# Optimization experiments

Hardware: AMD Instinct MI355X
Metric: run time of the kernel (lower is better)

## Reference

```python
import jax, jax.numpy as jnp
import numpy as np

B, T, D = 64, 512, 1024
H0, H1 = 1024, 1024

def setup_inputs() -> dict:
    key = jax.random.key(0)
    k1, k2, k3 = jax.random.split(key, 3)
    # scale weights ~ 1/sqrt(fan_in) so tanh doesn't saturate
    s0 = 1.0 / np.sqrt(H0 + D)
    s1 = 1.0 / np.sqrt(H1 + H0)
    return {
        "x": jax.random.normal(k1, (B, T, D), dtype=jnp.float32),
        "W0": jax.random.normal(k2, (H0 + D, H0), dtype=jnp.float32) * s0,
        "b0": jnp.zeros((H0,), dtype=jnp.float32),
        "W1": jax.random.normal(k3, (H1 + H0, H1), dtype=jnp.float32) * s1,
        "b1": jnp.zeros((H1,), dtype=jnp.float32),
    }

def reference(x, W0, b0, W1, b1):
    batch = x.shape[0]
    h0_init = jnp.zeros((batch, W0.shape[1]), dtype=x.dtype)
    h1_init = jnp.zeros((batch, W1.shape[1]), dtype=x.dtype)

    def step(carry, xt):
        h0, h1 = carry
        # layer 0: concat(prev hidden, input) -> dense -> tanh
        h0 = jnp.tanh(jnp.concatenate([h0, xt], axis=-1) @ W0 + b0)
        # layer 1 consumes layer 0 output
        h1 = jnp.tanh(jnp.concatenate([h1, h0], axis=-1) @ W1 + b1)
        return (h0, h1), h1

    xs = jnp.swapaxes(x, 0, 1)  # [T, B, D] time-major for scan
    (h0_f, h1_f), ys = jax.lax.scan(step, (h0_init, h1_init), xs)
    outputs = jnp.swapaxes(ys, 0, 1)  # [B, T, H1]
    final_state = jnp.concatenate([h0_f, h1_f], axis=-1)  # [B, H0+H1]
    return outputs, final_state
```

## Files before the change

### kernel.cpp

```cpp
#include <hip/hip_runtime.h>
#include <cmath>


typedef unsigned short u16;
typedef unsigned int   u32;
typedef unsigned long long u64;
typedef __bf16 bf16x8 __attribute__((ext_vector_type(8)));
typedef u16    u16x8  __attribute__((ext_vector_type(8)));
typedef u16    u16x4  __attribute__((ext_vector_type(4)));
typedef float  f32x4  __attribute__((ext_vector_type(4)));

constexpr int BB = 64;
constexpr int TT = 512;
constexpr size_t SLOT   = (size_t)64 * 1024;
constexpr size_t SLAB_B = SLOT * 2;

constexpr size_t OFF_W0T = 262144;
constexpr size_t OFF_W1T = OFF_W0T + (size_t)1024 * 2048 * 2;
constexpr size_t OFF_R   = OFF_W1T + (size_t)1024 * 2048 * 2;

constexpr int LDS_REQ = 159744;

__device__ inline u16 f2bf(float f) { return __builtin_bit_cast(u16, (__bf16)f); }
__device__ inline float bf2f(u16 v) { return (float)__builtin_bit_cast(__bf16, v); }
__device__ inline float fast_tanh(float x) {
  x = fminf(15.f, fmaxf(-15.f, x));
  float e = __expf(2.f * x);
  return (e - 1.f) * __builtin_amdgcn_rcpf(e + 1.f);
}

__global__ void zero_flags(unsigned* f) {
  int i = blockIdx.x * 256 + threadIdx.x;
  if (i < 3 * 512 * 32) f[i] = 0;
}

__global__ void transpose_w(const float* __restrict__ W0,
                            const float* __restrict__ W1,
                            u16* __restrict__ wt_base) {
  __shared__ float tile[64][65];
  int bi  = blockIdx.x;
  int mat = bi >> 9;
  int t   = bi & 511;
  int tk = t & 31, tn = t >> 5;
  const float* W = mat ? W1 : W0;
  u16* Wt = wt_base + (size_t)mat * 1024 * 2048;
  int K0 = tk * 64, N0 = tn * 64;
  int tid = threadIdx.x;
  {
    int c4 = (tid & 15) * 4;
    int r  = tid >> 4;
    for (int i = 0; i < 4; ++i) {
      int kl = r + i * 16;
      float4 v = *(const float4*)(W + (size_t)(K0 + kl) * 1024 + N0 + c4);
      tile[kl][c4 + 0] = v.x; tile[kl][c4 + 1] = v.y;
      tile[kl][c4 + 2] = v.z; tile[kl][c4 + 3] = v.w;
    }
  }
  __syncthreads();
  {
    int nl = tid >> 3;
    int kc = (tid & 7) * 8;
    for (int pass = 0; pass < 2; ++pass) {
      int n = nl + pass * 32;
      u16x8 o;
      #pragma unroll
      for (int z = 0; z < 8; ++z) o[z] = f2bf(tile[kc + z][n]);
      *(u16x8*)(Wt + (size_t)(N0 + n) * 2048 + K0 + kc) = o;
    }
  }
}

__global__ void xconv(const float* __restrict__ x, u16* __restrict__ xb) {
  int bi = blockIdx.x;
  int b = bi >> 9, t = bi & 511;
  const float* src = x + ((size_t)b * TT + t) * 1024;
  u16* dst = xb + ((size_t)t * BB + b) * 1024;
  int i = threadIdx.x * 4;
  float4 v = *(const float4*)(src + i);
  u16x4 o; o[0] = f2bf(v.x); o[1] = f2bf(v.y); o[2] = f2bf(v.z); o[3] = f2bf(v.w);
  *(u16x4*)(dst + i) = o;
}

__device__ inline void poll1(unsigned* p) {
  while (__hip_atomic_load(p, __ATOMIC_RELAXED, __HIP_MEMORY_SCOPE_SYSTEM) == 0u)
    __builtin_amdgcn_s_sleep(1);
}

template<bool COHA>
__device__ inline void mm8(const u16* Abase, const u16* bp, size_t aoff,
                           int gbase, int n15, f32x4& acc0, f32x4& acc1) {
  const u16* ap = Abase + aoff;
  #pragma unroll
  for (int ks = 0; ks < 8; ++ks) {
    bf16x8 a;
    if constexpr (COHA) {
      u64 lo = __hip_atomic_load((u64*)(ap + ks * 32),     __ATOMIC_RELAXED, __HIP_MEMORY_SCOPE_SYSTEM);
      u64 hi = __hip_atomic_load((u64*)(ap + ks * 32 + 4), __ATOMIC_RELAXED, __HIP_MEMORY_SCOPE_SYSTEM);
      union { u64 q2[2]; bf16x8 v; } un; un.q2[0] = lo; un.q2[1] = hi;
      a = un.v;
    } else {
      a = __builtin_bit_cast(bf16x8, *(const u16x8*)(ap + ks * 32));
    }
    int g = (gbase + 4 * ks) ^ n15;
    bf16x8 b0 = __builtin_bit_cast(bf16x8, *(const u16x8*)(bp + g * 8));
    bf16x8 b1 = __builtin_bit_cast(bf16x8, *(const u16x8*)(bp + 16 * 1024 + g * 8));
    acc0 = __builtin_amdgcn_mfma_f32_16x16x32_bf16(a, b0, acc0, 0, 0, 0);
    acc1 = __builtin_amdgcn_mfma_f32_16x16x32_bf16(a, b1, acc1, 0, 0, 0);
  }
}
__device__ inline void mmf8(const float* Ap, const u16* bp,
                            int gbase, int n15, f32x4& acc0, f32x4& acc1) {
  #pragma unroll
  for (int ks = 0; ks < 8; ++ks) {
    float4 v0 = *(const float4*)(Ap + ks * 32);
    float4 v1 = *(const float4*)(Ap + ks * 32 + 4);
    bf16x8 a;
    a[0]=(__bf16)v0.x; a[1]=(__bf16)v0.y; a[2]=(__bf16)v0.z; a[3]=(__bf16)v0.w;
    a[4]=(__bf16)v1.x; a[5]=(__bf16)v1.y; a[6]=(__bf16)v1.z; a[7]=(__bf16)v1.w;
    int g = (gbase + 4 * ks) ^ n15;
    bf16x8 b0 = __builtin_bit_cast(bf16x8, *(const u16x8*)(bp + g * 8));
    bf16x8 b1 = __builtin_bit_cast(bf16x8, *(const u16x8*)(bp + 16 * 1024 + g * 8));
    acc0 = __builtin_amdgcn_mfma_f32_16x16x32_bf16(a, b0, acc0, 0, 0, 0);
    acc1 = __builtin_amdgcn_mfma_f32_16x16x32_bf16(a, b1, acc1, 0, 0, 0);
  }
}

template<bool COH>
__global__ void __launch_bounds__(1024, 1)
rnn_seq(const float* __restrict__ x, const float* __restrict__ b0v,
        const float* __restrict__ b1v, float* __restrict__ out,
        unsigned* __restrict__ flags, const u16* __restrict__ W0t,
        const u16* __restrict__ W1t, u16* __restrict__ h0r,
        u16* __restrict__ h1r, u16* __restrict__ ur,
        const u16* __restrict__ xb, int use_xb) {
  constexpr int RMASK = COH ? 15 : 511;
  constexpr int UMASK = COH ? 31 : 511;
  constexpr int RING = 16, URING = 32;
  extern __shared__ u16 lds[];
  unsigned* fl_h0 = flags;
  unsigned* fl_h1 = flags + 512 * 32;
  unsigned* fl_u  = flags + 2 * 512 * 32;

  int wg = blockIdx.x, tid = threadIdx.x;
  int grp = wg >> 5, j = wg & 31;
  int n0 = j * 32;
  int lane = tid & 63, wave = tid >> 6;
  int rb = wave & 3, ksl = wave >> 2;
  int n15 = lane & 15, q = lane >> 4;
  int r0 = rb * 16;

  u16*   wlds = lds;
  float* scr  = (float*)((char*)lds + ((grp == 1) ? 131072 : 65536));
  u16*   hch  = (u16*)((char*)scr + 24576);
  u32*   uc   = (u32*)((char*)hch + 4096);

  {
    const u16* Wt = (grp == 1) ? W1t : W0t;
    int nh = (grp == 1) ? 2 : 1;
    for (int h = 0; h < nh; ++h) {
      int kb = (grp == 1) ? h * 1024 : (grp == 2 ? 1024 : 0);
      for (int idx = tid; idx < 32 * 128; idx += 1024) {
        int n = idx >> 7, g = idx & 127;
        u16x8 v = *(const u16x8*)(Wt + (size_t)(n0 + n) * 2048 + kb + g * 8);
        *(u16x8*)(wlds + h * 32768 + n * 1024 + ((g ^ (n & 15)) * 8)) = v;
      }
    }
  }
  __syncthreads();

  const size_t aoff = (size_t)(r0 + n15) * 1024 + ksl * 256 + q * 8;
  const int gbase = 32 * ksl + q;
  const u16* bp0 = wlds + n15 * 1024;
  const u16* bp1 = wlds + 32768 + n15 * 1024;

  float bia = 0.f, bib = 0.f;
  if (grp == 1) { bia = b1v[n0 + n15]; bib = b1v[n0 + n15 + 16]; }
  if (grp == 2) { bia = b0v[n0 + n15]; bib = b0v[n0 + n15 + 16]; }

  auto scr_write = [&](const f32x4& a0, const f32x4& a1) {
    int base = ((rb * 3 + ksl - 1) * 2) * 256 + (q * 4) * 16 + n15;
    #pragma unroll
    for (int i = 0; i < 4; ++i) scr[base + i * 16] = a0[i];
    #pragma unroll
    for (int i = 0; i < 4; ++i) scr[base + 256 + i * 16] = a1[i];
  };
  auto scr_sum = [&](f32x4& a0, f32x4& a1) {
    #pragma unroll
    for (int s = 0; s < 3; ++s) {
      int base = ((rb * 3 + s) * 2) * 256 + (q * 4) * 16 + n15;
      #pragma unroll
      for (int i = 0; i < 4; ++i) a0[i] += scr[base + i * 16];
      #pragma unroll
      for (int i = 0; i < 4; ++i) a1[i] += scr[base + 256 + i * 16];
    }
  };
  auto hch_write = [&](const f32x4& a0, const f32x4& a1, auto&& act) {
    #pragma unroll
    for (int i = 0; i < 4; ++i) {
      int b = r0 + q * 4 + i;
      hch[b * 32 + n15]      = f2bf(act(a0[i], 0));
      hch[b * 32 + n15 + 16] = f2bf(act(a1[i], 1));
    }
  };
  const int sb  = tid >> 4;
  const int scc = (tid & 15) * 2;
  auto ring_store = [&](u16* slab) {
    u32 v = ((u32*)hch)[tid];
    __hip_atomic_store((u32*)(slab + sb * 1024 + n0 + scc), v,
                       __ATOMIC_RELAXED, __HIP_MEMORY_SCOPE_SYSTEM);
  };

  const size_t FIN = (size_t)BB * TT * 1024;

  if (grp == 0) {
    for (int t = 0; t < TT; ++t) {
      if (tid < 32)      { if (t > 0)            poll1(&fl_h0[(t - 1) * 32 + tid]); }
      else if (tid < 64) {                       poll1(&fl_u [t * 32 + (tid - 32)]); }
      else if (tid < 96) { if (COH && t >= RING) poll1(&fl_h1[(t - RING) * 32 + (tid - 64)]); }
      __syncthreads();
      f32x4 acc0 = {0.f, 0.f, 0.f, 0.f}, acc1 = acc0;
      if (t > 0)
        mm8<COH>(h0r + (size_t)((t - 1) & RMASK) * SLOT, bp0, aoff, gbase, n15, acc0, acc1);
      {
        const u16* us = ur + (size_t)(t & UMASK) * SLOT;
        const u32* up = (const u32*)(us + sb * 1024 + n0 + scc);
        u32 v = COH ? __hip_atomic_load((u32*)up, __ATOMIC_RELAXED, __HIP_MEMORY_SCOPE_SYSTEM)
                    : *up;
        uc[tid] = v;
      }
      if (ksl > 0) scr_write(acc0, acc1);
      __syncthreads();
      if (ksl == 0) {
        scr_sum(acc0, acc1);
        hch_write(acc0, acc1, [&](float a, int tile) {
          int b = 0; (void)b;
          return a;
        });
        #pragma unroll
        for (int i = 0; i < 4; ++i) {
          int b = r0 + q * 4 + i;
          float u0 = bf2f(((u16*)uc)[b * 32 + n15]);
          float u1 = bf2f(((u16*)uc)[b * 32 + n15 + 16]);
          hch[b * 32 + n15]      = f2bf(fast_tanh(acc0[i] + u0));
          hch[b * 32 + n15 + 16] = f2bf(fast_tanh(acc1[i] + u1));
        }
      }
      __syncthreads();
      ring_store(h0r + (size_t)(t & RMASK) * SLOT);
      __syncthreads();
      if (tid == 0)
        __hip_atomic_store(&fl_h0[t * 32 + j], 1u, __ATOMIC_RELAXED, __HIP_MEMORY_SCOPE_SYSTEM);
      if (t == TT - 1) {
        u32 v = ((u32*)hch)[tid];
        float2 o; o.x = bf2f((u16)(v & 0xffff)); o.y = bf2f((u16)(v >> 16));
        *(float2*)&out[FIN + (size_t)sb * 2048 + n0 + scc] = o;
      }
    }
  } else if (grp == 1) {
    for (int t = 0; t < TT; ++t) {
      if (tid < 32) poll1(&fl_h0[t * 32 + tid]);
      __syncthreads();
      f32x4 acc0 = {0.f, 0.f, 0.f, 0.f}, acc1 = acc0;
      mm8<COH>(h0r + (size_t)(t & RMASK) * SLOT, bp1, aoff, gbase, n15, acc0, acc1);
      if (tid < 32 && t > 0) poll1(&fl_h1[(t - 1) * 32 + tid]);
      __syncthreads();
      if (t > 0)
        mm8<COH>(h1r + (size_t)((t - 1) & RMASK) * SLOT, bp0, aoff, gbase, n15, acc0, acc1);
      if (ksl > 0) scr_write(acc0, acc1);
      __syncthreads();
      if (ksl == 0) {
        scr_sum(acc0, acc1);
        #pragma unroll
        for (int i = 0; i < 4; ++i) {
          int b = r0 + q * 4 + i;
          hch[b * 32 + n15]      = f2bf(fast_tanh(acc0[i] + bia));
          hch[b * 32 + n15 + 16] = f2bf(fast_tanh(acc1[i] + bib));
        }
      }
      __syncthreads();
      ring_store(h1r + (size_t)(t & RMASK) * SLOT);
      __syncthreads();
      if (tid == 0)
        __hip_atomic_store(&fl_h1[t * 32 + j], 1u, __ATOMIC_RELAXED, __HIP_MEMORY_SCOPE_SYSTEM);
      {
        u32 v = ((u32*)hch)[tid];
        float2 o; o.x = bf2f((u16)(v & 0xffff)); o.y = bf2f((u16)(v >> 16));
        __builtin_nontemporal_store(o.x, &out[((size_t)sb * TT + t) * 1024 + n0 + scc]);
        __builtin_nontemporal_store(o.y, &out[((size_t)sb * TT + t) * 1024 + n0 + scc + 1]);
        if (t == TT - 1)
          *(float2*)&out[FIN + (size_t)sb * 2048 + 1024 + n0 + scc] = o;
      }
    }
  } else {
    for (int t = 0; t < TT; ++t) {
      if (COH && t >= URING) {
        if (tid < 32) poll1(&fl_h0[(t - URING) * 32 + tid]);
      }
      __syncthreads();
      f32x4 acc0 = {0.f, 0.f, 0.f, 0.f}, acc1 = acc0;
      if (use_xb) {
        mm8<false>(xb + (size_t)t * SLOT, bp0, aoff, gbase, n15, acc0, acc1);
      } else {
        const float* Ap = x + ((size_t)(r0 + n15) * TT + t) * 1024 + ksl * 256 + q * 8;
        mmf8(Ap, bp0, gbase, n15, acc0, acc1);
      }
      if (ksl > 0) scr_write(acc0, acc1);
      __syncthreads();
      if (ksl == 0) {
        scr_sum(acc0, acc1);
        #pragma unroll
        for (int i = 0; i < 4; ++i) {
          int b = r0 + q * 4 + i;
          hch[b * 32 + n15]      = f2bf(acc0[i] + bia);
          hch[b * 32 + n15 + 16] = f2bf(acc1[i] + bib);
        }
      }
      __syncthreads();
      ring_store(ur + (size_t)(t & UMASK) * SLOT);
      __syncthreads();
      if (tid == 0)
        __hip_atomic_store(&fl_u[t * 32 + j], 1u, __ATOMIC_RELAXED, __HIP_MEMORY_SCOPE_SYSTEM);
    }
  }
}

extern "C" void kernel_launch(void* const* d_in, const int* in_sizes, int n_in,
                              void* d_out, int out_size, void* d_ws, size_t ws_size,
                              hipStream_t stream) {
  const float* x  = (const float*)d_in[0];
  const float* W0 = (const float*)d_in[1];
  const float* b0 = (const float*)d_in[2];
  const float* W1 = (const float*)d_in[3];
  const float* b1 = (const float*)d_in[4];
  float* out = (float*)d_out;
  unsigned char* ws = (unsigned char*)d_ws;

  const size_t WS_PLAIN = OFF_R + 4ull * 512 * SLAB_B;
  bool plain = ws_size >= WS_PLAIN;
  size_t nslot  = plain ? 512 : 16;
  size_t nuslot = plain ? 512 : 32;
  size_t o_h0 = OFF_R;
  size_t o_h1 = o_h0 + nslot  * SLAB_B;
  size_t o_u  = o_h1 + nslot  * SLAB_B;
  size_t o_xb = o_u  + nuslot * SLAB_B;
  int use_xb = (plain || ws_size >= o_xb + (size_t)TT * SLAB_B) ? 1 : 0;

  unsigned* flags = (unsigned*)ws;
  const u16* W0t = (const u16*)(ws + OFF_W0T);
  const u16* W1t = (const u16*)(ws + OFF_W1T);
  u16* h0r = (u16*)(ws + o_h0);
  u16* h1r = (u16*)(ws + o_h1);
  u16* ur  = (u16*)(ws + o_u);
  u16* xb  = (u16*)(ws + o_xb);

  zero_flags<<<192, 256, 0, stream>>>(flags);
  transpose_w<<<1024, 256, 0, stream>>>(W0, W1, (u16*)(ws + OFF_W0T));
  if (use_xb) xconv<<<32768, 256, 0, stream>>>(x, xb);

  (void)hipFuncSetAttribute((const void*)rnn_seq<false>,
                            hipFuncAttributeMaxDynamicSharedMemorySize, LDS_REQ);
  (void)hipFuncSetAttribute((const void*)rnn_seq<true>,
                            hipFuncAttributeMaxDynamicSharedMemorySize, LDS_REQ);

  void* args[12];
  args[0]  = (void*)&x;    args[1]  = (void*)&b0;   args[2]  = (void*)&b1;
  args[3]  = (void*)&out;  args[4]  = (void*)&flags;
  args[5]  = (void*)&W0t;  args[6]  = (void*)&W1t;
  args[7]  = (void*)&h0r;  args[8]  = (void*)&h1r;  args[9]  = (void*)&ur;
  args[10] = (void*)&xb;   args[11] = (void*)&use_xb;
  hipLaunchCooperativeKernel(plain ? (void*)rnn_seq<false> : (void*)rnn_seq<true>,
                             dim3(96), dim3(1024), args, LDS_REQ, stream);
}
```

Before: 4.649 ms.

## Reorder layer-1 dependency waits and batch A-operand loads before MFMAs

Splits the matmul helper into a load phase that fetches all eight A fragments into registers and a separate MFMA phase, so the loads can be issued together and their latency overlapped. In group 0 the h0 fragment loads are issued before the u-slab read. In group 1 the order of the two dependencies is swapped: the recurrent h1(t-1) product is computed first, before waiting on the h0(t) flag, which takes that half of the work off the critical path behind layer 0. This costs more live registers, which could raise register pressure at 1024 threads per block.

```diff
diff --git a/kernel.cpp b/kernel.cpp
--- a/kernel.cpp
+++ b/kernel.cpp
@@ -87,41 +87,30 @@
 }
 
 template<bool COHA>
-__device__ inline void mm8(const u16* Abase, const u16* bp, size_t aoff,
-                           int gbase, int n15, f32x4& acc0, f32x4& acc1) {
+__device__ inline void load_a8(const u16* Abase, size_t aoff, bf16x8* a) {
   const u16* ap = Abase + aoff;
   #pragma unroll
   for (int ks = 0; ks < 8; ++ks) {
-    bf16x8 a;
     if constexpr (COHA) {
       u64 lo = __hip_atomic_load((u64*)(ap + ks * 32),     __ATOMIC_RELAXED, __HIP_MEMORY_SCOPE_SYSTEM);
       u64 hi = __hip_atomic_load((u64*)(ap + ks * 32 + 4), __ATOMIC_RELAXED, __HIP_MEMORY_SCOPE_SYSTEM);
       union { u64 q2[2]; bf16x8 v; } un; un.q2[0] = lo; un.q2[1] = hi;
-      a = un.v;
+      a[ks] = un.v;
     } else {
-      a = __builtin_bit_cast(bf16x8, *(const u16x8*)(ap + ks * 32));
-    }
+      a[ks] = __builtin_bit_cast(bf16x8, *(const u16x8*)(ap + ks * 32));
+    }
+  }
+}
+
+__device__ inline void fma8(const bf16x8* a, const u16* bp,
+                            int gbase, int n15, f32x4& acc0, f32x4& acc1) {
+  #pragma unroll
+  for (int ks = 0; ks < 8; ++ks) {
     int g = (gbase + 4 * ks) ^ n15;
     bf16x8 b0 = __builtin_bit_cast(bf16x8, *(const u16x8*)(bp + g * 8));
     bf16x8 b1 = __builtin_bit_cast(bf16x8, *(const u16x8*)(bp + 16 * 1024 + g * 8));
-    acc0 = __builtin_amdgcn_mfma_f32_16x16x32_bf16(a, b0, acc0, 0, 0, 0);
-    acc1 = __builtin_amdgcn_mfma_f32_16x16x32_bf16(a, b1, acc1, 0, 0, 0);
-  }
-}
-__device__ inline void mmf8(const float* Ap, const u16* bp,
-                            int gbase, int n15, f32x4& acc0, f32x4& acc1) {
-  #pragma unroll
-  for (int ks = 0; ks < 8; ++ks) {
-    float4 v0 = *(const float4*)(Ap + ks * 32);
-    float4 v1 = *(const float4*)(Ap + ks * 32 + 4);
-    bf16x8 a;
-    a[0]=(__bf16)v0.x; a[1]=(__bf16)v0.y; a[2]=(__bf16)v0.z; a[3]=(__bf16)v0.w;
-    a[4]=(__bf16)v1.x; a[5]=(__bf16)v1.y; a[6]=(__bf16)v1.z; a[7]=(__bf16)v1.w;
-    int g = (gbase + 4 * ks) ^ n15;
-    bf16x8 b0 = __builtin_bit_cast(bf16x8, *(const u16x8*)(bp + g * 8));
-    bf16x8 b1 = __builtin_bit_cast(bf16x8, *(const u16x8*)(bp + 16 * 1024 + g * 8));
-    acc0 = __builtin_amdgcn_mfma_f32_16x16x32_bf16(a, b0, acc0, 0, 0, 0);
-    acc1 = __builtin_amdgcn_mfma_f32_16x16x32_bf16(a, b1, acc1, 0, 0, 0);
+    acc0 = __builtin_amdgcn_mfma_f32_16x16x32_bf16(a[ks], b0, acc0, 0, 0, 0);
+    acc1 = __builtin_amdgcn_mfma_f32_16x16x32_bf16(a[ks], b1, acc1, 0, 0, 0);
   }
 }
 
@@ -194,14 +183,6 @@
       for (int i = 0; i < 4; ++i) a1[i] += scr[base + 256 + i * 16];
     }
   };
-  auto hch_write = [&](const f32x4& a0, const f32x4& a1, auto&& act) {
-    #pragma unroll
-    for (int i = 0; i < 4; ++i) {
-      int b = r0 + q * 4 + i;
-      hch[b * 32 + n15]      = f2bf(act(a0[i], 0));
-      hch[b * 32 + n15 + 16] = f2bf(act(a1[i], 1));
-    }
-  };
   const int sb  = tid >> 4;
   const int scc = (tid & 15) * 2;
   auto ring_store = [&](u16* slab) {
@@ -218,9 +199,8 @@
       else if (tid < 64) {                       poll1(&fl_u [t * 32 + (tid - 32)]); }
       else if (tid < 96) { if (COH && t >= RING) poll1(&fl_h1[(t - RING) * 32 + (tid - 64)]); }
       __syncthreads();
-      f32x4 acc0 = {0.f, 0.f, 0.f, 0.f}, acc1 = acc0;
-      if (t > 0)
-        mm8<COH>(h0r + (size_t)((t - 1) & RMASK) * SLOT, bp0, aoff, gbase, n15, acc0, acc1);
+      bf16x8 a[8];
+      if (t > 0) load_a8<COH>(h0r + (size_t)((t - 1) & RMASK) * SLOT, aoff, a);
       {
         const u16* us = ur + (size_t)(t & UMASK) * SLOT;
         const u32* up = (const u32*)(us + sb * 1024 + n0 + scc);
@@ -228,14 +208,12 @@
                     : *up;
         uc[tid] = v;
       }
+      f32x4 acc0 = {0.f, 0.f, 0.f, 0.f}, acc1 = acc0;
+      if (t > 0) fma8(a, bp0, gbase, n15, acc0, acc1);
       if (ksl > 0) scr_write(acc0, acc1);
       __syncthreads();
       if (ksl == 0) {
         scr_sum(acc0, acc1);
-        hch_write(acc0, acc1, [&](float a, int tile) {
-          int b = 0; (void)b;
-          return a;
-        });
         #pragma unroll
         for (int i = 0; i < 4; ++i) {
           int b = r0 + q * 4 + i;
@@ -258,14 +236,21 @@
     }
   } else if (grp == 1) {
     for (int t = 0; t < TT; ++t) {
+      if (tid < 32 && t > 0) poll1(&fl_h1[(t - 1) * 32 + tid]);
+      __syncthreads();
+      f32x4 acc0 = {0.f, 0.f, 0.f, 0.f}, acc1 = acc0;
+      if (t > 0) {
+        bf16x8 a1[8];
+        load_a8<COH>(h1r + (size_t)((t - 1) & RMASK) * SLOT, aoff, a1);
+        fma8(a1, bp0, gbase, n15, acc0, acc1);
+      }
       if (tid < 32) poll1(&fl_h0[t * 32 + tid]);
       __syncthreads();
-      f32x4 acc0 = {0.f, 0.f, 0.f, 0.f}, acc1 = acc0;
-      mm8<COH>(h0r + (size_t)(t & RMASK) * SLOT, bp1, aoff, gbase, n15, acc0, acc1);
-      if (tid < 32 && t > 0) poll1(&fl_h1[(t - 1) * 32 + tid]);
-      __syncthreads();
-      if (t > 0)
-        mm8<COH>(h1r + (size_t)((t - 1) & RMASK) * SLOT, bp0, aoff, gbase, n15, acc0, acc1);
+      {
+        bf16x8 a0[8];
+        load_a8<COH>(h0r + (size_t)(t & RMASK) * SLOT, aoff, a0);
+        fma8(a0, bp1, gbase, n15, acc0, acc1);
+      }
       if (ksl > 0) scr_write(acc0, acc1);
       __syncthreads();
       if (ksl == 0) {
@@ -298,12 +283,28 @@
       }
       __syncthreads();
       f32x4 acc0 = {0.f, 0.f, 0.f, 0.f}, acc1 = acc0;
+      bf16x8 a[8];
       if (use_xb) {
-        mm8<false>(xb + (size_t)t * SLOT, bp0, aoff, gbase, n15, acc0, acc1);
+        load_a8<false>(xb + (size_t)t * SLOT, aoff, a);
       } else {
         const float* Ap = x + ((size_t)(r0 + n15) * TT + t) * 1024 + ksl * 256 + q * 8;
-        mmf8(Ap, bp0, gbase, n15, acc0, acc1);
-      }
+        float4 f[16];
+        #pragma unroll
+        for (int ks = 0; ks < 8; ++ks) {
+          f[2 * ks]     = *(const float4*)(Ap + ks * 32);
+          f[2 * ks + 1] = *(const float4*)(Ap + ks * 32 + 4);
+        }
+        #pragma unroll
+        for (int ks = 0; ks < 8; ++ks) {
+          bf16x8 tv;
+          tv[0] = (__bf16)f[2*ks].x;   tv[1] = (__bf16)f[2*ks].y;
+          tv[2] = (__bf16)f[2*ks].z;   tv[3] = (__bf16)f[2*ks].w;
+          tv[4] = (__bf16)f[2*ks+1].x; tv[5] = (__bf16)f[2*ks+1].y;
+          tv[6] = (__bf16)f[2*ks+1].z; tv[7] = (__bf16)f[2*ks+1].w;
+          a[ks] = tv;
+        }
+      }
+      fma8(a, bp0, gbase, n15, acc0, acc1);
       if (ksl > 0) scr_write(acc0, acc1);
       __syncthreads();
       if (ksl == 0) {
```

After: 4.889 ms. 5.2% more time.
